# Performance work log

Hardware: AMD Instinct MI355X
Metric: run time of the kernel (lower is better)

## Reference

```python
import jax, jax.numpy as jnp
import numpy as np

N_NODES = 100000
N_EDGES = 800000
N_IN = 256
N_H = 128


def setup_inputs() -> dict:
    key = jax.random.key(0)
    ks = jax.random.split(key, 8)
    x_1 = jax.random.normal(ks[0], (1, N_NODES, N_IN), dtype=jnp.float32)
    x_2 = jax.random.normal(ks[1], (1, N_NODES, N_IN), dtype=jnp.float32)
    edge_index = jax.random.randint(ks[2], (2, N_EDGES), 0, N_NODES, dtype=jnp.int32)
    edge_weight = jax.random.uniform(ks[3], (N_EDGES,), dtype=jnp.float32)
    # xavier-uniform-ish init for fc weight (stored as [in, out])
    lim = float(np.sqrt(6.0 / (N_IN + N_H)))
    W_gcn = jax.random.uniform(ks[4], (N_IN, N_H), minval=-lim, maxval=lim, dtype=jnp.float32)
    gcn_bias = jnp.zeros((N_H,), dtype=jnp.float32)
    prelu_a = jnp.full((1,), 0.25, dtype=jnp.float32)  # PReLU default slope
    lim2 = float(np.sqrt(1.0 / N_H))
    lin_W = jax.random.uniform(ks[5], (N_H, N_H), minval=-lim2, maxval=lim2, dtype=jnp.float32)
    lin_b = jax.random.uniform(ks[6], (N_H,), minval=-lim2, maxval=lim2, dtype=jnp.float32)
    return {
        "x_1": x_1, "x_2": x_2, "edge_index": edge_index, "edge_weight": edge_weight,
        "W_gcn": W_gcn, "gcn_bias": gcn_bias, "prelu_a": prelu_a,
        "lin_W": lin_W, "lin_b": lin_b,
    }


def _prelu(x, a):
    return jnp.where(x >= 0, x, a * x)


def _gcn(feat, edge_index, edge_weight, W, b, a, n_nodes):
    # feat: [1, N, n_in] -> h: [N, n_h]
    h = jnp.squeeze(feat, 0) @ W
    row, col = edge_index[0], edge_index[1]
    # spmm: out[i] = sum_{e: row_e = i} w_e * h[col_e]
    msg = edge_weight[:, None] * h[col]            # [E, n_h]
    agg = jax.ops.segment_sum(msg, row, num_segments=n_nodes)  # [N, n_h]
    return _prelu(agg + b, a)                      # [N, n_h]


def reference(x_1, x_2, edge_index, edge_weight, W_gcn, gcn_bias, prelu_a, lin_W, lin_b):
    n = x_1.shape[1]
    h_1 = _gcn(x_1, edge_index, edge_weight, W_gcn, gcn_bias, prelu_a, n)
    h_2 = _gcn(x_2, edge_index, edge_weight, W_gcn, gcn_bias, prelu_a, n)
    z_1 = (h_1 @ lin_W + lin_b).sum(1)   # [N]
    z_2 = (h_2 @ lin_W + lin_b).sum(1)   # [N]
    return jnp.concatenate((z_1, z_2), 0)  # [2N]
```

## Files before the change

kernel.cpp:

```cpp
#include <hip/hip_runtime.h>

#define N_NODES 100000
#define N_EDGES 800000
#define N_IN    256
#define N_H     128
#define M_TOT   (2 * N_NODES)

typedef __bf16 bfx8 __attribute__((ext_vector_type(8)));
typedef unsigned short u16x8 __attribute__((ext_vector_type(8)));
typedef float fx4 __attribute__((ext_vector_type(4)));

__device__ inline unsigned short f2bf(float f) {
    union { float f; unsigned u; } v; v.f = f;
    return (unsigned short)((v.u + 0x7FFF + ((v.u >> 16) & 1)) >> 16);
}
__device__ inline float bf2f(unsigned short s) {
    union { unsigned u; float f; } v; v.u = ((unsigned)s) << 16;
    return v.f;
}

__device__ inline void async16(const void* g, void* l) {
    __builtin_amdgcn_global_load_lds((const __attribute__((address_space(1))) void*)g,
                                     (__attribute__((address_space(3))) void*)l, 16, 0, 0);
}

#define NT    12500
#define NTB1  6250
#define NSB2  3125
#define NGB2  1024

__global__ __launch_bounds__(256, 4) void gemm_scatter_kernel(
        const float* __restrict__ x1, const float* __restrict__ x2,
        const unsigned short* __restrict__ wT,
        unsigned short* __restrict__ hb,
        const int* __restrict__ ei, const float* __restrict__ ew,
        int* __restrict__ cursor, int2* __restrict__ edata) {
    const int t = threadIdx.x;
    if (blockIdx.x < NSB2) {
        int e = blockIdx.x * 256 + t;
        int row = ei[e];
        int pos = atomicAdd(cursor + row, 1);
        edata[pos] = make_int2(ei[N_EDGES + e] << 8, __float_as_int(ew[e]));
        return;
    }
    __shared__ __align__(16) float Abuf[2][16][256];
    const int wv = t >> 6, ln = t & 63;
    const int quad = ln >> 4, l16 = ln & 15, sw = l16 & 7;

#define STAGE(buf, TT) do {                                                    \
        int br_ = (TT) >= NTB1;                                                \
        const float* xs_ = br_ ? x2 : x1;                                      \
        const float* base_ = xs_ + (size_t)((TT) - br_ * NTB1) * (16 * N_IN);  \
        _Pragma("unroll")                                                      \
        for (int i_ = 0; i_ < 4; ++i_) {                                       \
            int r_ = wv * 4 + i_;                                              \
            async16(base_ + (size_t)r_ * N_IN + ((ln ^ (r_ & 7)) << 2),        \
                    &Abuf[(buf)][r_][0]);                                      \
        }                                                                      \
    } while (0)

    int T = blockIdx.x - NSB2;
    STAGE(0, T);

    bfx8 Bf[2][8];
#pragma unroll
    for (int c2 = 0; c2 < 2; ++c2)
#pragma unroll
        for (int kc = 0; kc < 8; ++kc)
            Bf[c2][kc] = *(const bfx8*)(wT +
                (size_t)(wv * 32 + c2 * 16 + l16) * N_IN + kc * 32 + quad * 8);

    int cur = 0;
    for (; T < NT; T += NGB2) {
        int Tn = T + NGB2;
        if (Tn < NT) {
            STAGE(cur ^ 1, Tn);
            asm volatile("s_waitcnt vmcnt(4)" ::: "memory");
        } else {
            asm volatile("s_waitcnt vmcnt(0)" ::: "memory");
        }
        asm volatile("s_barrier" ::: "memory");
        {
            int br = T >= NTB1;
            int node0 = (T - br * NTB1) * 16;
            fx4 acc0 = {0.f, 0.f, 0.f, 0.f}, acc1 = {0.f, 0.f, 0.f, 0.f};
            const float* rowp = &Abuf[cur][l16][0];
#pragma unroll
            for (int kc = 0; kc < 8; ++kc) {
                int s0 = kc * 8 + quad * 2;
                fx4 lo = *(const fx4*)(rowp + (((s0    ) ^ sw) << 2));
                fx4 hi = *(const fx4*)(rowp + (((s0 + 1) ^ sw) << 2));
                u16x8 au;
                au[0] = f2bf(lo[0]); au[1] = f2bf(lo[1]);
                au[2] = f2bf(lo[2]); au[3] = f2bf(lo[3]);
                au[4] = f2bf(hi[0]); au[5] = f2bf(hi[1]);
                au[6] = f2bf(hi[2]); au[7] = f2bf(hi[3]);
                bfx8 af = __builtin_bit_cast(bfx8, au);
                acc0 = __builtin_amdgcn_mfma_f32_16x16x32_bf16(af, Bf[0][kc], acc0, 0, 0, 0);
                acc1 = __builtin_amdgcn_mfma_f32_16x16x32_bf16(af, Bf[1][kc], acc1, 0, 0, 0);
            }
            unsigned short* hp = hb + (size_t)node0 * 256 + br * 128 + wv * 32 + l16;
#pragma unroll
            for (int r = 0; r < 4; ++r) {
                size_t off = (size_t)(quad * 4 + r) * 256;
                hp[off]      = f2bf(acc0[r]);
                hp[off + 16] = f2bf(acc1[r]);
            }
        }
        asm volatile("s_barrier" ::: "memory");
        cur ^= 1;
    }
#undef STAGE
}

#define HIST_BLKS 3125
__global__ __launch_bounds__(256) void prep_kernel(const int* __restrict__ ei,
                                                   int* __restrict__ deg,
                                                   const float* __restrict__ W,
                                                   unsigned short* __restrict__ wT,
                                                   const float* __restrict__ linW,
                                                   const float* __restrict__ linb,
                                                   float* __restrict__ wsum) {
    const int t = threadIdx.x;
    if (blockIdx.x < HIST_BLKS) {
        int e = blockIdx.x * 256 + t;
        if (e < N_EDGES) atomicAdd(deg + ei[e], 1);
    } else if (blockIdx.x < HIST_BLKS + 32) {
        int kb = (blockIdx.x - HIST_BLKS) * 8;
#pragma unroll
        for (int p = 0; p < 4; ++p) {
            int idx = p * 256 + t;
            int k = kb + (idx >> 7), n = idx & 127;
            wT[(size_t)n * N_IN + k] = f2bf(W[(size_t)k * N_H + n]);
        }
    } else {
        int j = t;
        if (j < N_H) {
            float s = 0.f;
            for (int o = 0; o < N_H; ++o) s += linW[j * N_H + o];
            wsum[j] = s;
        }
        if (j == N_H) {
            float s = 0.f;
            for (int o = 0; o < N_H; ++o) s += linb[o];
            wsum[N_H] = s;
        }
    }
}

__global__ __launch_bounds__(256) void scan1_kernel(const int* __restrict__ deg,
                                                    int* __restrict__ part,
                                                    int* __restrict__ bsum) {
    __shared__ int s[256];
    int g = blockIdx.x * 256 + threadIdx.x;
    int v = (g < N_NODES) ? deg[g] : 0;
    s[threadIdx.x] = v;
    __syncthreads();
#pragma unroll
    for (int off = 1; off < 256; off <<= 1) {
        int t = (threadIdx.x >= off) ? s[threadIdx.x - off] : 0;
        __syncthreads();
        s[threadIdx.x] += t;
        __syncthreads();
    }
    if (g < N_NODES) part[g] = s[threadIdx.x] - v;
    if (threadIdx.x == 255) bsum[blockIdx.x] = s[255];
}

#define NBLK_SCAN 391
__global__ void scan2_kernel(int* __restrict__ bsum) {
    __shared__ int s[512];
    int v = (threadIdx.x < NBLK_SCAN) ? bsum[threadIdx.x] : 0;
    s[threadIdx.x] = v;
    __syncthreads();
#pragma unroll
    for (int off = 1; off < 512; off <<= 1) {
        int t = (threadIdx.x >= off) ? s[threadIdx.x - off] : 0;
        __syncthreads();
        s[threadIdx.x] += t;
        __syncthreads();
    }
    if (threadIdx.x < NBLK_SCAN) bsum[threadIdx.x] = s[threadIdx.x] - v;
}

__global__ __launch_bounds__(256) void scan3_kernel(const int* __restrict__ part,
                                                    const int* __restrict__ bsum,
                                                    int* __restrict__ off,
                                                    int* __restrict__ cursor) {
    int g = blockIdx.x * 256 + threadIdx.x;
    if (g < N_NODES) {
        int o = part[g] + bsum[blockIdx.x];
        off[g] = o;
        cursor[g] = o;
    }
    if (g == 0) off[N_NODES] = N_EDGES;
}

__global__ __launch_bounds__(256) void gcn_seg_kernel(const int* __restrict__ off,
                                                      const int2* __restrict__ edata,
                                                      const unsigned short* __restrict__ hb,
                                                      const float* __restrict__ gcn_bias,
                                                      const float* __restrict__ prelu_a,
                                                      const float* __restrict__ wsum,
                                                      float* __restrict__ zout) {
    const int wave = threadIdx.x >> 6, lane = threadIdx.x & 63;
    const int node = blockIdx.x * 4 + wave;
    const int s = __builtin_amdgcn_readfirstlane(off[node]);
    const int e = __builtin_amdgcn_readfirstlane(off[node + 1]);
    const int l2 = lane * 2;
    float a0 = 0.f, a1 = 0.f;
    float b0 = 0.f, b1 = 0.f;
    int i = s;
    for (; i + 1 < e; i += 2) {
        int2 E0 = edata[i], E1 = edata[i + 1];
        float w0 = __int_as_float(E0.y), w1 = __int_as_float(E1.y);
        ushort2 p10 = *(const ushort2*)(hb + E0.x + l2);
        ushort2 p20 = *(const ushort2*)(hb + E0.x + 128 + l2);
        ushort2 p11 = *(const ushort2*)(hb + E1.x + l2);
        ushort2 p21 = *(const ushort2*)(hb + E1.x + 128 + l2);
        a0 += w0 * bf2f(p10.x) + w1 * bf2f(p11.x);
        a1 += w0 * bf2f(p10.y) + w1 * bf2f(p11.y);
        b0 += w0 * bf2f(p20.x) + w1 * bf2f(p21.x);
        b1 += w0 * bf2f(p20.y) + w1 * bf2f(p21.y);
    }
    if (i < e) {
        int2 E0 = edata[i];
        float w0 = __int_as_float(E0.y);
        ushort2 p10 = *(const ushort2*)(hb + E0.x + l2);
        ushort2 p20 = *(const ushort2*)(hb + E0.x + 128 + l2);
        a0 += w0 * bf2f(p10.x);
        a1 += w0 * bf2f(p10.y);
        b0 += w0 * bf2f(p20.x);
        b1 += w0 * bf2f(p20.y);
    }
    const float alpha = prelu_a[0];
    const float g0 = gcn_bias[l2], g1 = gcn_bias[l2 + 1];
    const float q0 = wsum[l2],     q1 = wsum[l2 + 1];
    float v0 = a0 + g0, v1 = a1 + g1;
    float u0 = b0 + g0, u1 = b1 + g1;
    v0 = (v0 >= 0.f) ? v0 : alpha * v0;
    v1 = (v1 >= 0.f) ? v1 : alpha * v1;
    u0 = (u0 >= 0.f) ? u0 : alpha * u0;
    u1 = (u1 >= 0.f) ? u1 : alpha * u1;
    float s1 = v0 * q0 + v1 * q1;
    float s2 = u0 * q0 + u1 * q1;
#pragma unroll
    for (int o = 32; o; o >>= 1) {
        s1 += __shfl_down(s1, o, 64);
        s2 += __shfl_down(s2, o, 64);
    }
    if (lane == 0) {
        zout[node]           = s1 + wsum[128];
        zout[node + N_NODES] = s2 + wsum[128];
    }
}

extern "C" void kernel_launch(void* const* d_in, const int* in_sizes, int n_in,
                              void* d_out, int out_size, void* d_ws, size_t ws_size,
                              hipStream_t stream) {
    const float* x1 = (const float*)d_in[0];
    const float* x2 = (const float*)d_in[1];
    const int*   ei = (const int*)d_in[2];
    const float* ew = (const float*)d_in[3];
    const float* Wg = (const float*)d_in[4];
    const float* gb = (const float*)d_in[5];
    const float* pa = (const float*)d_in[6];
    const float* lW = (const float*)d_in[7];
    const float* lb = (const float*)d_in[8];
    float* zout = (float*)d_out;

    unsigned short* hb   = (unsigned short*)d_ws;
    int2*  edata  = (int2*)(hb + (size_t)M_TOT * N_H);
    unsigned short* wT   = (unsigned short*)(edata + N_EDGES);
    int*   deg    = (int*)(wT + N_IN * N_H);
    int*   part   = deg + 100096;
    int*   off    = part + 100096;
    int*   cursor = off + 100096;
    int*   bsum   = cursor + 100096;
    float* wsum   = (float*)(bsum + 512);

    hipMemsetAsync(deg, 0, (size_t)N_NODES * sizeof(int), stream);
    prep_kernel<<<HIST_BLKS + 33, 256, 0, stream>>>(ei, deg, Wg, wT, lW, lb, wsum);
    scan1_kernel<<<NBLK_SCAN, 256, 0, stream>>>(deg, part, bsum);
    scan2_kernel<<<1, 512, 0, stream>>>(bsum);
    scan3_kernel<<<NBLK_SCAN, 256, 0, stream>>>(part, bsum, off, cursor);
    gemm_scatter_kernel<<<NSB2 + NGB2, 256, 0, stream>>>(x1, x2, wT, hb,
                                                         ei, ew, cursor, edata);
    gcn_seg_kernel<<<N_NODES / 4, 256, 0, stream>>>(off, edata, hb, gb, pa, wsum, zout);
}
```

Baseline: 387.3 us.

## Split edge scatter from GEMM kernel and use native bf16 conversions

Splits the fused scatter+GEMM launch into a separate edge-scatter kernel followed by a standalone GEMM kernel. It also replaces the manual round-to-nearest-even float-to-bf16 bit arithmetic with native __bf16 casts, which may map to hardware conversion instructions. An empty asm constraint pins the preloaded B fragments in registers. The split is meant to stop the GEMM blocks from sharing the GPU with atomic-heavy scatter blocks, at the cost of an extra launch and losing the overlap between the two phases.

```diff
diff --git a/kernel.cpp b/kernel.cpp
--- a/kernel.cpp
+++ b/kernel.cpp
@@ -24,26 +24,26 @@
                                      (__attribute__((address_space(3))) void*)l, 16, 0, 0);
 }
 
+#define NSB2  3125
+__global__ __launch_bounds__(256) void scatter_kernel(
+        const int* __restrict__ ei, const float* __restrict__ ew,
+        int* __restrict__ cursor, int2* __restrict__ edata) {
+    int e = blockIdx.x * 256 + threadIdx.x;
+    int row = ei[e];
+    int pos = atomicAdd(cursor + row, 1);
+    edata[pos] = make_int2(ei[N_EDGES + e] << 8, __float_as_int(ew[e]));
+}
+
 #define NT    12500
 #define NTB1  6250
-#define NSB2  3125
-#define NGB2  1024
-
-__global__ __launch_bounds__(256, 4) void gemm_scatter_kernel(
+#define NGB3  1024
+
+__global__ __launch_bounds__(256, 4) void gemm_kernel(
         const float* __restrict__ x1, const float* __restrict__ x2,
         const unsigned short* __restrict__ wT,
-        unsigned short* __restrict__ hb,
-        const int* __restrict__ ei, const float* __restrict__ ew,
-        int* __restrict__ cursor, int2* __restrict__ edata) {
+        unsigned short* __restrict__ hb) {
+    __shared__ __align__(16) float Abuf[2][16][256];
     const int t = threadIdx.x;
-    if (blockIdx.x < NSB2) {
-        int e = blockIdx.x * 256 + t;
-        int row = ei[e];
-        int pos = atomicAdd(cursor + row, 1);
-        edata[pos] = make_int2(ei[N_EDGES + e] << 8, __float_as_int(ew[e]));
-        return;
-    }
-    __shared__ __align__(16) float Abuf[2][16][256];
     const int wv = t >> 6, ln = t & 63;
     const int quad = ln >> 4, l16 = ln & 15, sw = l16 & 7;
 
@@ -59,7 +59,7 @@
         }                                                                      \
     } while (0)
 
-    int T = blockIdx.x - NSB2;
+    int T = blockIdx.x;
     STAGE(0, T);
 
     bfx8 Bf[2][8];
@@ -69,10 +69,15 @@
         for (int kc = 0; kc < 8; ++kc)
             Bf[c2][kc] = *(const bfx8*)(wT +
                 (size_t)(wv * 32 + c2 * 16 + l16) * N_IN + kc * 32 + quad * 8);
+#pragma unroll
+    for (int c2 = 0; c2 < 2; ++c2)
+#pragma unroll
+        for (int kc = 0; kc < 8; ++kc)
+            asm volatile("" : "+v"(Bf[c2][kc]));
 
     int cur = 0;
-    for (; T < NT; T += NGB2) {
-        int Tn = T + NGB2;
+    for (; T < NT; T += NGB3) {
+        int Tn = T + NGB3;
         if (Tn < NT) {
             STAGE(cur ^ 1, Tn);
             asm volatile("s_waitcnt vmcnt(4)" ::: "memory");
@@ -90,12 +95,11 @@
                 int s0 = kc * 8 + quad * 2;
                 fx4 lo = *(const fx4*)(rowp + (((s0    ) ^ sw) << 2));
                 fx4 hi = *(const fx4*)(rowp + (((s0 + 1) ^ sw) << 2));
-                u16x8 au;
-                au[0] = f2bf(lo[0]); au[1] = f2bf(lo[1]);
-                au[2] = f2bf(lo[2]); au[3] = f2bf(lo[3]);
-                au[4] = f2bf(hi[0]); au[5] = f2bf(hi[1]);
-                au[6] = f2bf(hi[2]); au[7] = f2bf(hi[3]);
-                bfx8 af = __builtin_bit_cast(bfx8, au);
+                bfx8 af;
+                af[0] = (__bf16)lo[0]; af[1] = (__bf16)lo[1];
+                af[2] = (__bf16)lo[2]; af[3] = (__bf16)lo[3];
+                af[4] = (__bf16)hi[0]; af[5] = (__bf16)hi[1];
+                af[6] = (__bf16)hi[2]; af[7] = (__bf16)hi[3];
                 acc0 = __builtin_amdgcn_mfma_f32_16x16x32_bf16(af, Bf[0][kc], acc0, 0, 0, 0);
                 acc1 = __builtin_amdgcn_mfma_f32_16x16x32_bf16(af, Bf[1][kc], acc1, 0, 0, 0);
             }
@@ -103,8 +107,8 @@
 #pragma unroll
             for (int r = 0; r < 4; ++r) {
                 size_t off = (size_t)(quad * 4 + r) * 256;
-                hp[off]      = f2bf(acc0[r]);
-                hp[off + 16] = f2bf(acc1[r]);
+                hp[off]      = __builtin_bit_cast(unsigned short, (__bf16)acc0[r]);
+                hp[off + 16] = __builtin_bit_cast(unsigned short, (__bf16)acc1[r]);
             }
         }
         asm volatile("s_barrier" ::: "memory");
@@ -284,7 +288,7 @@
     scan1_kernel<<<NBLK_SCAN, 256, 0, stream>>>(deg, part, bsum);
     scan2_kernel<<<1, 512, 0, stream>>>(bsum);
     scan3_kernel<<<NBLK_SCAN, 256, 0, stream>>>(part, bsum, off, cursor);
-    gemm_scatter_kernel<<<NSB2 + NGB2, 256, 0, stream>>>(x1, x2, wT, hb,
-                                                         ei, ew, cursor, edata);
+    scatter_kernel<<<NSB2, 256, 0, stream>>>(ei, ew, cursor, edata);
+    gemm_kernel<<<NGB3, 256, 0, stream>>>(x1, x2, wT, hb);
     gcn_seg_kernel<<<N_NODES / 4, 256, 0, stream>>>(off, edata, hb, gb, pa, wsum, zout);
 }
```

After: 393.0 us. No clear change (+1.5%).
